# Optimization experiments

Measured on AMD Instinct MI355X. Metric: run time of the kernel, lower is better.

## Reference

```python
import jax, jax.numpy as jnp
import numpy as np

SLOPE = 25.0   # fast_sigmoid surrogate slope
THR = 1.0      # snntorch Leaky default threshold


@jax.custom_vjp
def spike(x):
    # Heaviside forward, fast-sigmoid surrogate backward
    return (x > 0).astype(x.dtype)

def _spike_fwd(x):
    return spike(x), x

def _spike_bwd(x, g):
    return (g / (SLOPE * jnp.abs(x) + 1.0) ** 2,)

spike.defvjp(_spike_fwd, _spike_bwd)


def conv2d(x, w, b):
    y = jax.lax.conv_general_dilated(
        x, w, window_strides=(1, 1), padding=((1, 1), (1, 1)),
        dimension_numbers=('NCHW', 'OIHW', 'NCHW'))
    return y + b[None, :, None, None]


def maxpool2(x):
    return jax.lax.reduce_window(x, -jnp.inf, jax.lax.max,
                                 (1, 1, 2, 2), (1, 1, 2, 2), 'VALID')


def bn_inf(x, g, b, m, v):
    # inference-mode BatchNorm2d, eps = 1e-5
    inv = g * jax.lax.rsqrt(v + 1e-5)
    return x * inv[None, :, None, None] + (b - m * inv)[None, :, None, None]


def lif_step(mem, inp, beta):
    # snntorch Leaky, reset_mechanism='subtract', learn_beta (clamped to [0,1])
    b = jnp.clip(beta, 0.0, 1.0)
    reset = jax.lax.stop_gradient((mem > THR).astype(mem.dtype))
    mem_new = b * mem + inp - reset * THR
    spk = spike(mem_new - THR)
    return spk, mem_new


def setup_inputs() -> dict:
    key = jax.random.key(0)
    ks = jax.random.split(key, 20)
    T, B, H, W = 25, 512, 100, 64   # T steps, batch, MAX_LEN, N_MELS
    NUM_CLASSES = 35
    FLAT = 32 * (H // 4) * (W // 4)  # 12800
    f32 = jnp.float32
    inp = {
        'x': jax.random.normal(ks[0], (T, B, H, W), f32),
        'conv1_w': jax.random.normal(ks[1], (16, 1, 3, 3), f32) * 0.2,
        'conv1_b': jnp.zeros((16,), f32),
        'bn1_g': jnp.ones((16,), f32),
        'bn1_b': jnp.zeros((16,), f32),
        'bn1_m': jax.random.normal(ks[2], (16,), f32) * 0.1,
        'bn1_v': jax.random.uniform(ks[3], (16,), f32) + 0.5,
        'conv2_w': jax.random.normal(ks[4], (32, 16, 3, 3), f32) * (1.0 / np.sqrt(16 * 9)),
        'conv2_b': jnp.zeros((32,), f32),
        'bn2_g': jnp.ones((32,), f32),
        'bn2_b': jnp.zeros((32,), f32),
        'bn2_m': jax.random.normal(ks[5], (32,), f32) * 0.1,
        'bn2_v': jax.random.uniform(ks[6], (32,), f32) + 0.5,
        'fc1_w': jax.random.normal(ks[7], (256, FLAT), f32) * (1.0 / np.sqrt(FLAT)),
        'fc1_b': jnp.zeros((256,), f32),
        'fc2_w': jax.random.normal(ks[8], (128, 256), f32) * (1.0 / np.sqrt(256)),
        'fc2_b': jnp.zeros((128,), f32),
        'fc3_w': jax.random.normal(ks[9], (NUM_CLASSES, 128), f32) * (1.0 / np.sqrt(128)),
        'fc3_b': jnp.zeros((NUM_CLASSES,), f32),
        'beta1': jnp.float32(0.9),
        'beta2': jnp.float32(0.9),
        'beta3': jnp.float32(0.9),
    }
    return inp


def reference(x, conv1_w, conv1_b, bn1_g, bn1_b, bn1_m, bn1_v,
              conv2_w, conv2_b, bn2_g, bn2_b, bn2_m, bn2_v,
              fc1_w, fc1_b, fc2_w, fc2_b, fc3_w, fc3_b,
              beta1, beta2, beta3):
    T, B = x.shape[0], x.shape[1]
    # CNN runs once on the time-averaged input
    x_mean = jnp.mean(x, axis=0)[:, None]          # (B, 1, H, W)
    f = maxpool2(jax.nn.relu(bn_inf(conv2d(x_mean, conv1_w, conv1_b), bn1_g, bn1_b, bn1_m, bn1_v)))
    f = maxpool2(jax.nn.relu(bn_inf(conv2d(f, conv2_w, conv2_b), bn2_g, bn2_b, bn2_m, bn2_v)))
    feat = f.reshape(B, -1)                        # (B, FLAT)
    # fc1 input is the same every step (dropout = identity in eval)
    cur1 = feat @ fc1_w.T + fc1_b                  # (B, 256)

    m1 = jnp.zeros((B, fc1_w.shape[0]), x.dtype)
    m2 = jnp.zeros((B, fc2_w.shape[0]), x.dtype)
    m3 = jnp.zeros((B, fc3_w.shape[0]), x.dtype)

    def step(carry, _):
        m1, m2, m3 = carry
        spk1, m1 = lif_step(m1, cur1, beta1)
        spk2, m2 = lif_step(m2, spk1 @ fc2_w.T + fc2_b, beta2)
        spk3, m3 = lif_step(m3, spk2 @ fc3_w.T + fc3_b, beta3)
        return (m1, m2, m3), spk3

    _, out = jax.lax.scan(step, (m1, m2, m3), None, length=T)
    return out                                     # (T, B, NUM_CLASSES)
```

## Files before the change

### kernel.cpp

```cpp
#include <hip/hip_runtime.h>

#define N_P1    (512*16*50*32)
#define N_FEAT  (512*12800)
#define N_PART  (32*512*256)

#define WS_P1    0
#define WS_FEAT  (WS_P1 + N_P1)
#define WS_PART  (WS_FEAT + N_FEAT)
#define WS_S1    0
#define WS_IN2   3276800
#define WS_S2    4915200
#define WS_IN3   6553600

__global__ __launch_bounds__(384) void conv1_kernel(const float* __restrict__ x,
                                                    const float* __restrict__ w1,
                                                    const float* __restrict__ cb1,
                                                    const float* __restrict__ g1,
                                                    const float* __restrict__ bb1,
                                                    const float* __restrict__ m1g,
                                                    const float* __restrict__ v1,
                                                    float* __restrict__ p1) {
    __shared__ float xs[22 * 66];
    __shared__ float w1s[144];
    __shared__ float sh1s[16];
    const int b = blockIdx.x, s = blockIdx.y;
    const int tid = threadIdx.x;
    if (tid < 144) {
        int c = tid / 9;
        float inv = g1[c] * rsqrtf(v1[c] + 1e-5f);
        w1s[tid] = w1[tid] * inv;
    }
    if (tid >= 144 && tid < 160) {
        int c = tid - 144;
        float inv = g1[c] * rsqrtf(v1[c] + 1e-5f);
        sh1s[c] = cb1[c] * inv + bb1[c] - m1g[c] * inv;
    }
    if (tid >= 160 && tid < 204) {
        int q = tid - 160;
        xs[(q >> 1) * 66 + (q & 1) * 65] = 0.f;
    }
    const int r0 = s * 20 - 1;
    const size_t TSTR = (size_t)512 * 6400;
    if (tid < 352) {
        int lr = tid >> 4, cq = tid & 15;
        int gr = r0 + lr;
        float4 a0 = make_float4(0.f, 0.f, 0.f, 0.f), a1 = a0, a2 = a0, a3 = a0;
        if (gr >= 0 && gr < 100) {
            const float* px = x + (size_t)b * 6400 + gr * 64 + cq * 4;
            #pragma unroll
            for (int tt = 0; tt < 24; tt += 4) {
                float4 v0 = *(const float4*)(px + (size_t)(tt + 0) * TSTR);
                float4 v1_ = *(const float4*)(px + (size_t)(tt + 1) * TSTR);
                float4 v2_ = *(const float4*)(px + (size_t)(tt + 2) * TSTR);
                float4 v3 = *(const float4*)(px + (size_t)(tt + 3) * TSTR);
                a0.x += v0.x; a0.y += v0.y; a0.z += v0.z; a0.w += v0.w;
                a1.x += v1_.x; a1.y += v1_.y; a1.z += v1_.z; a1.w += v1_.w;
                a2.x += v2_.x; a2.y += v2_.y; a2.z += v2_.z; a2.w += v2_.w;
                a3.x += v3.x; a3.y += v3.y; a3.z += v3.z; a3.w += v3.w;
            }
            float4 v = *(const float4*)(px + (size_t)24 * TSTR);
            a0.x += v.x; a0.y += v.y; a0.z += v.z; a0.w += v.w;
        }
        const float sc = 1.0f / 25.0f;
        float* d = &xs[lr * 66 + 1 + cq * 4];
        d[0] = (a0.x + a1.x + a2.x + a3.x) * sc;
        d[1] = (a0.y + a1.y + a2.y + a3.y) * sc;
        d[2] = (a0.z + a1.z + a2.z + a3.z) * sc;
        d[3] = (a0.w + a1.w + a2.w + a3.w) * sc;
    }
    __syncthreads();
    if (tid < 320) {
        int phl = tid >> 5, pw = tid & 31;
        int ph = s * 10 + phl;
        float win[4][4];
        #pragma unroll
        for (int a = 0; a < 4; ++a)
            #pragma unroll
            for (int c2 = 0; c2 < 4; ++c2)
                win[a][c2] = xs[(2 * phl + a) * 66 + 2 * pw + c2];
        #pragma unroll 1
        for (int c = 0; c < 16; ++c) {
            float s00 = 0.f, s01 = 0.f, s10 = 0.f, s11 = 0.f;
            #pragma unroll
            for (int dh = 0; dh < 3; ++dh)
                #pragma unroll
                for (int dw = 0; dw < 3; ++dw) {
                    float w = w1s[c * 9 + dh * 3 + dw];
                    s00 = fmaf(win[dh][dw],         w, s00);
                    s01 = fmaf(win[dh][dw + 1],     w, s01);
                    s10 = fmaf(win[dh + 1][dw],     w, s10);
                    s11 = fmaf(win[dh + 1][dw + 1], w, s11);
                }
            float m = fmaxf(fmaxf(s00, s01), fmaxf(s10, s11));
            float val = fmaxf(m + sh1s[c], 0.f);
            p1[(((size_t)b * 16 + c) * 50 + ph) * 32 + pw] = val;
        }
    }
}

__global__ __launch_bounds__(320) void conv2_kernel(const float* __restrict__ p1,
                                                    const float* __restrict__ w2g,
                                                    const float* __restrict__ cb2,
                                                    const float* __restrict__ g2,
                                                    const float* __restrict__ bb2,
                                                    const float* __restrict__ m2g,
                                                    const float* __restrict__ v2,
                                                    float* __restrict__ feat) {
    __shared__ float ins[16 * 12 * 36];
    __shared__ float wl[16 * 9 * 32];
    __shared__ float sh2s[32];
    const int b = blockIdx.x, s = blockIdx.y;
    const int tid = threadIdx.x;
    const int chg = tid & 15, q = (tid >> 4) & 3, phl = tid >> 6;
    const int ph = s * 5 + phl;

    for (int i = tid; i < 192; i += 320) {
        int ci = i / 12, lr = i - ci * 12;
        int gr = s * 10 - 1 + lr;
        float* dst = &ins[(ci * 12 + lr) * 36];
        if (gr >= 0 && gr < 50) {
            const float* src = p1 + (((size_t)b * 16 + ci) * 50 + gr) * 32;
            float4 v0 = *(const float4*)src;
            dst[0] = 0.f; dst[1] = v0.x; dst[2] = v0.y; dst[3] = v0.z;
            #pragma unroll
            for (int qq = 1; qq < 8; ++qq) {
                float4 v = *(const float4*)(src + 4 * qq - 1);
                *(float4*)(dst + 4 * qq) = v;
            }
            dst[32] = src[31];
            dst[33] = 0.f; dst[34] = 0.f; dst[35] = 0.f;
        } else {
            #pragma unroll
            for (int qq = 0; qq < 9; ++qq) *(float4*)(dst + 4 * qq) = make_float4(0.f, 0.f, 0.f, 0.f);
        }
    }
    for (int i = tid; i < 4608; i += 320) {
        int c = i / 144, rem = i - c * 144;
        float inv = g2[c] * rsqrtf(v2[c] + 1e-5f);
        wl[rem * 32 + c] = w2g[i] * inv;
    }
    if (tid < 32) {
        float inv = g2[tid] * rsqrtf(v2[tid] + 1e-5f);
        sh2s[tid] = cb2[tid] * inv + bb2[tid] - m2g[tid] * inv;
    }
    __syncthreads();

    float acc[2][2][8];
    #pragma unroll
    for (int c = 0; c < 2; ++c)
        #pragma unroll
        for (int a = 0; a < 2; ++a)
            #pragma unroll
            for (int xx = 0; xx < 8; ++xx) acc[c][a][xx] = 0.f;
    const int xb = q * 8;
    #pragma unroll 1
    for (int ci = 0; ci < 16; ++ci) {
        float2 wv[9];
        #pragma unroll
        for (int t = 0; t < 9; ++t)
            wv[t] = *(const float2*)&wl[(ci * 9 + t) * 32 + 2 * chg];
        #pragma unroll
        for (int lr4 = 0; lr4 < 4; ++lr4) {
            const float* row = &ins[(ci * 12 + (2 * phl + lr4)) * 36 + xb];
            float v[10];
            float4 t0 = *(const float4*)&row[0];
            float4 t1 = *(const float4*)&row[4];
            float2 t2 = *(const float2*)&row[8];
            v[0]=t0.x; v[1]=t0.y; v[2]=t0.z; v[3]=t0.w;
            v[4]=t1.x; v[5]=t1.y; v[6]=t1.z; v[7]=t1.w;
            v[8]=t2.x; v[9]=t2.y;
            #pragma unroll
            for (int a = 0; a < 2; ++a) {
                const int dh = lr4 - a;
                if (dh >= 0 && dh <= 2) {
                    #pragma unroll
                    for (int dw = 0; dw < 3; ++dw) {
                        float w0 = wv[dh * 3 + dw].x;
                        float w1 = wv[dh * 3 + dw].y;
                        #pragma unroll
                        for (int xx = 0; xx < 8; ++xx) {
                            acc[0][a][xx] = fmaf(v[xx + dw], w0, acc[0][a][xx]);
                            acc[1][a][xx] = fmaf(v[xx + dw], w1, acc[1][a][xx]);
                        }
                    }
                }
            }
        }
    }
    #pragma unroll
    for (int ch = 0; ch < 2; ++ch) {
        const int c = 2 * chg + ch;
        const float sh = sh2s[c];
        #pragma unroll
        for (int p = 0; p < 4; ++p) {
            float m = fmaxf(fmaxf(acc[ch][0][2 * p], acc[ch][0][2 * p + 1]),
                            fmaxf(acc[ch][1][2 * p], acc[ch][1][2 * p + 1]));
            float val = fmaxf(m + sh, 0.f);
            feat[(((size_t)b * 32 + c) * 25 + ph) * 16 + q * 4 + p] = val;
        }
    }
}

__global__ __launch_bounds__(256) void fc1_kernel(const float* __restrict__ feat,
                                                  const float* __restrict__ w,
                                                  float* __restrict__ part) {
    __shared__ float As[16 * 136];
    __shared__ float Bs[16 * 136];
    const int bx = blockIdx.x, by = blockIdx.y, bz = blockIdx.z;
    const int tid = threadIdx.x;
    const int tm = tid >> 4, tn = tid & 15;
    const int r = tid >> 2, cq = tid & 3;
    const int m0 = bx * 128, n0 = by * 128;
    const size_t aBase = (size_t)(m0 + r) * 12800 + bz * 400 + cq * 4;
    const size_t bBase = (size_t)(n0 + r) * 12800 + bz * 400 + cq * 4;
    float acc[8][8] = {};
    float4 a0 = *(const float4*)(feat + aBase);
    float4 a1 = *(const float4*)(feat + aBase + (size_t)64 * 12800);
    float4 b0 = *(const float4*)(w    + bBase);
    float4 b1 = *(const float4*)(w    + bBase + (size_t)64 * 12800);

    for (int kt = 0; kt < 25; ++kt) {
        __syncthreads();
        As[(cq * 4 + 0) * 136 + r]      = a0.x; As[(cq * 4 + 1) * 136 + r]      = a0.y;
        As[(cq * 4 + 2) * 136 + r]      = a0.z; As[(cq * 4 + 3) * 136 + r]      = a0.w;
        As[(cq * 4 + 0) * 136 + 64 + r] = a1.x; As[(cq * 4 + 1) * 136 + 64 + r] = a1.y;
        As[(cq * 4 + 2) * 136 + 64 + r] = a1.z; As[(cq * 4 + 3) * 136 + 64 + r] = a1.w;
        Bs[(cq * 4 + 0) * 136 + r]      = b0.x; Bs[(cq * 4 + 1) * 136 + r]      = b0.y;
        Bs[(cq * 4 + 2) * 136 + r]      = b0.z; Bs[(cq * 4 + 3) * 136 + r]      = b0.w;
        Bs[(cq * 4 + 0) * 136 + 64 + r] = b1.x; Bs[(cq * 4 + 1) * 136 + 64 + r] = b1.y;
        Bs[(cq * 4 + 2) * 136 + 64 + r] = b1.z; Bs[(cq * 4 + 3) * 136 + 64 + r] = b1.w;
        __syncthreads();
        if (kt < 24) {
            const int o = (kt + 1) * 16;
            a0 = *(const float4*)(feat + aBase + o);
            a1 = *(const float4*)(feat + aBase + (size_t)64 * 12800 + o);
            b0 = *(const float4*)(w    + bBase + o);
            b1 = *(const float4*)(w    + bBase + (size_t)64 * 12800 + o);
        }
        #pragma unroll
        for (int kk = 0; kk < 16; ++kk) {
            float4 av0 = *(const float4*)&As[kk * 136 + tm * 8];
            float4 av1 = *(const float4*)&As[kk * 136 + tm * 8 + 4];
            float4 bv0 = *(const float4*)&Bs[kk * 136 + tn * 8];
            float4 bv1 = *(const float4*)&Bs[kk * 136 + tn * 8 + 4];
            float a_[8] = {av0.x, av0.y, av0.z, av0.w, av1.x, av1.y, av1.z, av1.w};
            float b_[8] = {bv0.x, bv0.y, bv0.z, bv0.w, bv1.x, bv1.y, bv1.z, bv1.w};
            #pragma unroll
            for (int i = 0; i < 8; ++i)
                #pragma unroll
                for (int j = 0; j < 8; ++j)
                    acc[i][j] = fmaf(a_[i], b_[j], acc[i][j]);
        }
    }
    #pragma unroll
    for (int i = 0; i < 8; ++i) {
        float* dst = &part[(size_t)bz * 131072 + (size_t)(m0 + tm * 8 + i) * 256 + n0 + tn * 8];
        *(float4*)dst       = make_float4(acc[i][0], acc[i][1], acc[i][2], acc[i][3]);
        *(float4*)(dst + 4) = make_float4(acc[i][4], acc[i][5], acc[i][6], acc[i][7]);
    }
}

__global__ __launch_bounds__(256) void lif1_kernel(const float* __restrict__ part,
                                                   const float* __restrict__ b1g,
                                                   const float* __restrict__ pb1,
                                                   float* __restrict__ S1) {
    const int i = blockIdx.x * 256 + threadIdx.x;
    const int k = i & 255;
    float cu = b1g[k];
    #pragma unroll 8
    for (int z = 0; z < 32; ++z) cu += part[(size_t)z * 131072 + i];
    const float be = fminf(fmaxf(pb1[0], 0.f), 1.f);
    float m = 0.f;
    #pragma unroll
    for (int t = 0; t < 25; ++t) {
        float r = (m > 1.f) ? 1.f : 0.f;
        m = fmaf(be, m, cu) - r;
        S1[(size_t)t * 131072 + i] = (m > 1.f) ? 1.f : 0.f;
    }
}

__global__ __launch_bounds__(256) void fc2g_kernel(const float* __restrict__ S1,
                                                   const float* __restrict__ w2g,
                                                   const float* __restrict__ b2g,
                                                   float* __restrict__ in2) {
    __shared__ float As[16 * 36];
    __shared__ float Bs[16 * 136];
    const int m0 = blockIdx.x * 32;
    const int tid = threadIdx.x;
    const int tm = tid >> 4, tn = tid & 15;
    const int ra = tid >> 2, cqa = tid & 3;
    const int rb = tid >> 1, kb = (tid & 1) * 8;
    float acc[2][8] = {};
    float4 av = make_float4(0.f, 0.f, 0.f, 0.f);
    if (tid < 128) av = *(const float4*)&S1[(size_t)(m0 + ra) * 256 + cqa * 4];
    float4 bv0 = *(const float4*)&w2g[rb * 256 + kb];
    float4 bv1 = *(const float4*)&w2g[rb * 256 + kb + 4];

    for (int kt = 0; kt < 16; ++kt) {
        __syncthreads();
        if (tid < 128) {
            As[(cqa * 4 + 0) * 36 + ra] = av.x; As[(cqa * 4 + 1) * 36 + ra] = av.y;
            As[(cqa * 4 + 2) * 36 + ra] = av.z; As[(cqa * 4 + 3) * 36 + ra] = av.w;
        }
        Bs[(kb + 0) * 136 + rb] = bv0.x; Bs[(kb + 1) * 136 + rb] = bv0.y;
        Bs[(kb + 2) * 136 + rb] = bv0.z; Bs[(kb + 3) * 136 + rb] = bv0.w;
        Bs[(kb + 4) * 136 + rb] = bv1.x; Bs[(kb + 5) * 136 + rb] = bv1.y;
        Bs[(kb + 6) * 136 + rb] = bv1.z; Bs[(kb + 7) * 136 + rb] = bv1.w;
        __syncthreads();
        if (kt < 15) {
            const int o = (kt + 1) * 16;
            if (tid < 128) av = *(const float4*)&S1[(size_t)(m0 + ra) * 256 + o + cqa * 4];
            bv0 = *(const float4*)&w2g[rb * 256 + o + kb];
            bv1 = *(const float4*)&w2g[rb * 256 + o + kb + 4];
        }
        #pragma unroll
        for (int kk = 0; kk < 16; ++kk) {
            float2 a2 = *(const float2*)&As[kk * 36 + tm * 2];
            float4 bw0 = *(const float4*)&Bs[kk * 136 + tn * 8];
            float4 bw1 = *(const float4*)&Bs[kk * 136 + tn * 8 + 4];
            float b_[8] = {bw0.x, bw0.y, bw0.z, bw0.w, bw1.x, bw1.y, bw1.z, bw1.w};
            #pragma unroll
            for (int j = 0; j < 8; ++j) {
                acc[0][j] = fmaf(a2.x, b_[j], acc[0][j]);
                acc[1][j] = fmaf(a2.y, b_[j], acc[1][j]);
            }
        }
    }
    float4 bb0 = *(const float4*)&b2g[tn * 8];
    float4 bb1 = *(const float4*)&b2g[tn * 8 + 4];
    #pragma unroll
    for (int i = 0; i < 2; ++i) {
        float* dst = &in2[(size_t)(m0 + tm * 2 + i) * 128 + tn * 8];
        *(float4*)dst       = make_float4(acc[i][0] + bb0.x, acc[i][1] + bb0.y,
                                          acc[i][2] + bb0.z, acc[i][3] + bb0.w);
        *(float4*)(dst + 4) = make_float4(acc[i][4] + bb1.x, acc[i][5] + bb1.y,
                                          acc[i][6] + bb1.z, acc[i][7] + bb1.w);
    }
}

__global__ __launch_bounds__(256) void lif2_kernel(const float* __restrict__ in2,
                                                   const float* __restrict__ pb2,
                                                   float* __restrict__ S2) {
    const int i = blockIdx.x * 256 + threadIdx.x;
    const float be = fminf(fmaxf(pb2[0], 0.f), 1.f);
    float m = 0.f;
    #pragma unroll
    for (int t = 0; t < 25; ++t) {
        float r = (m > 1.f) ? 1.f : 0.f;
        m = fmaf(be, m, in2[(size_t)t * 65536 + i]) - r;
        S2[(size_t)t * 65536 + i] = (m > 1.f) ? 1.f : 0.f;
    }
}

__global__ __launch_bounds__(256) void fc3g_kernel(const float* __restrict__ S2,
                                                   const float* __restrict__ w3g,
                                                   const float* __restrict__ b3g,
                                                   float* __restrict__ in3) {
    __shared__ float As[16 * 36];
    __shared__ float Bs[16 * 48];
    const int m0 = blockIdx.x * 32;
    const int tid = threadIdx.x;
    const int tm = tid >> 4, tn = tid & 15;
    float acc[2][3] = {};
    for (int kt = 0; kt < 8; ++kt) {
        __syncthreads();
        if (tid < 128) {
            int r = tid >> 2, cq = tid & 3;
            float4 av = *(const float4*)&S2[(size_t)(m0 + r) * 128 + kt * 16 + cq * 4];
            As[(cq * 4 + 0) * 36 + r] = av.x; As[(cq * 4 + 1) * 36 + r] = av.y;
            As[(cq * 4 + 2) * 36 + r] = av.z; As[(cq * 4 + 3) * 36 + r] = av.w;
        }
        for (int i = tid; i < 560; i += 256) {
            int kk = i / 35, c = i - kk * 35;
            Bs[kk * 48 + c] = w3g[c * 128 + kt * 16 + kk];
        }
        __syncthreads();
        #pragma unroll
        for (int kk = 0; kk < 16; ++kk) {
            float2 a2 = *(const float2*)&As[kk * 36 + tm * 2];
            float w0 = Bs[kk * 48 + tn];
            float w1 = Bs[kk * 48 + tn + 16];
            float w2 = Bs[kk * 48 + tn + 32];
            acc[0][0] = fmaf(a2.x, w0, acc[0][0]); acc[1][0] = fmaf(a2.y, w0, acc[1][0]);
            acc[0][1] = fmaf(a2.x, w1, acc[0][1]); acc[1][1] = fmaf(a2.y, w1, acc[1][1]);
            acc[0][2] = fmaf(a2.x, w2, acc[0][2]); acc[1][2] = fmaf(a2.y, w2, acc[1][2]);
        }
    }
    const float bias0 = b3g[tn];
    const float bias1 = b3g[tn + 16];
    const float bias2 = (tn < 3) ? b3g[tn + 32] : 0.f;
    #pragma unroll
    for (int i = 0; i < 2; ++i) {
        const size_t row = (size_t)(m0 + tm * 2 + i) * 35;
        in3[row + tn]      = acc[i][0] + bias0;
        in3[row + tn + 16] = acc[i][1] + bias1;
        if (tn < 3) in3[row + tn + 32] = acc[i][2] + bias2;
    }
}

__global__ __launch_bounds__(256) void lif3_kernel(const float* __restrict__ in3,
                                                   const float* __restrict__ pb3,
                                                   float* __restrict__ out) {
    const int i = blockIdx.x * 256 + threadIdx.x;
    if (i >= 17920) return;
    const float be = fminf(fmaxf(pb3[0], 0.f), 1.f);
    float m = 0.f;
    #pragma unroll
    for (int t = 0; t < 25; ++t) {
        float r = (m > 1.f) ? 1.f : 0.f;
        m = fmaf(be, m, in3[(size_t)t * 17920 + i]) - r;
        out[(size_t)t * 17920 + i] = (m > 1.f) ? 1.f : 0.f;
    }
}

extern "C" void kernel_launch(void* const* d_in, const int* in_sizes, int n_in,
                              void* d_out, int out_size, void* d_ws, size_t ws_size,
                              hipStream_t stream) {
    const float* x     = (const float*)d_in[0];
    const float* c1w   = (const float*)d_in[1];
    const float* c1b   = (const float*)d_in[2];
    const float* bn1g  = (const float*)d_in[3];
    const float* bn1b  = (const float*)d_in[4];
    const float* bn1m  = (const float*)d_in[5];
    const float* bn1v  = (const float*)d_in[6];
    const float* c2w   = (const float*)d_in[7];
    const float* c2b   = (const float*)d_in[8];
    const float* bn2g  = (const float*)d_in[9];
    const float* bn2b  = (const float*)d_in[10];
    const float* bn2m  = (const float*)d_in[11];
    const float* bn2v  = (const float*)d_in[12];
    const float* fc1w  = (const float*)d_in[13];
    const float* fc1b  = (const float*)d_in[14];
    const float* fc2w  = (const float*)d_in[15];
    const float* fc2b  = (const float*)d_in[16];
    const float* fc3w  = (const float*)d_in[17];
    const float* fc3b  = (const float*)d_in[18];
    const float* beta1 = (const float*)d_in[19];
    const float* beta2 = (const float*)d_in[20];
    const float* beta3 = (const float*)d_in[21];
    float* ws  = (float*)d_ws;
    float* out = (float*)d_out;

    conv1_kernel<<<dim3(512, 5), 384, 0, stream>>>(x, c1w, c1b, bn1g, bn1b, bn1m, bn1v,
                                                   ws + WS_P1);
    conv2_kernel<<<dim3(512, 5), 320, 0, stream>>>(ws + WS_P1, c2w, c2b, bn2g, bn2b, bn2m, bn2v,
                                                   ws + WS_FEAT);
    fc1_kernel<<<dim3(4, 2, 32), 256, 0, stream>>>(ws + WS_FEAT, fc1w, ws + WS_PART);
    lif1_kernel<<<512, 256, 0, stream>>>(ws + WS_PART, fc1b, beta1, ws + WS_S1);
    fc2g_kernel<<<400, 256, 0, stream>>>(ws + WS_S1, fc2w, fc2b, ws + WS_IN2);
    lif2_kernel<<<256, 256, 0, stream>>>(ws + WS_IN2, beta2, ws + WS_S2);
    fc3g_kernel<<<400, 256, 0, stream>>>(ws + WS_S2, fc3w, fc3b, ws + WS_IN3);
    lif3_kernel<<<70, 256, 0, stream>>>(ws + WS_IN3, beta3, out);
}
```

Baseline: 300.4 us.

## Retile fc1 to full-N 128x256 tiles with 64-way split-K, nontemporal input loads

The fc1 GEMM now gives each block a full 256-wide N tile with a 16x8 micro-tile per thread. K is split 64 ways (200 per block) instead of 32, so the launch stays at 256 blocks while each feature row is read once per block rather than twice. The B shared-memory layout is padded (stride 10 per 8 columns) to reduce bank conflicts. conv1 reads the large time-series input with nontemporal vector loads to avoid polluting cache, and the workspace layout is reshuffled to hold the larger partial buffer. The costs are 64 partial sums to reduce in lif1, more registers per thread (launch bounds set to one block), and more partial-sum memory traffic.

```diff
diff --git a/kernel.cpp b/kernel.cpp
--- a/kernel.cpp
+++ b/kernel.cpp
@@ -1,16 +1,14 @@
 #include <hip/hip_runtime.h>
 
-#define N_P1    (512*16*50*32)
-#define N_FEAT  (512*12800)
-#define N_PART  (32*512*256)
+typedef float f4nt __attribute__((ext_vector_type(4)));
 
 #define WS_P1    0
-#define WS_FEAT  (WS_P1 + N_P1)
-#define WS_PART  (WS_FEAT + N_FEAT)
-#define WS_S1    0
-#define WS_IN2   3276800
-#define WS_S2    4915200
-#define WS_IN3   6553600
+#define WS_FEAT  13107200
+#define WS_PART  0
+#define WS_S1    8388608
+#define WS_IN2   11665408
+#define WS_S2    13303808
+#define WS_IN3   14942208
 
 __global__ __launch_bounds__(384) void conv1_kernel(const float* __restrict__ x,
                                                     const float* __restrict__ w1,
@@ -44,29 +42,24 @@
     if (tid < 352) {
         int lr = tid >> 4, cq = tid & 15;
         int gr = r0 + lr;
-        float4 a0 = make_float4(0.f, 0.f, 0.f, 0.f), a1 = a0, a2 = a0, a3 = a0;
+        f4nt a0 = {0.f, 0.f, 0.f, 0.f}, a1 = a0, a2 = a0, a3 = a0;
         if (gr >= 0 && gr < 100) {
             const float* px = x + (size_t)b * 6400 + gr * 64 + cq * 4;
             #pragma unroll
             for (int tt = 0; tt < 24; tt += 4) {
-                float4 v0 = *(const float4*)(px + (size_t)(tt + 0) * TSTR);
-                float4 v1_ = *(const float4*)(px + (size_t)(tt + 1) * TSTR);
-                float4 v2_ = *(const float4*)(px + (size_t)(tt + 2) * TSTR);
-                float4 v3 = *(const float4*)(px + (size_t)(tt + 3) * TSTR);
-                a0.x += v0.x; a0.y += v0.y; a0.z += v0.z; a0.w += v0.w;
-                a1.x += v1_.x; a1.y += v1_.y; a1.z += v1_.z; a1.w += v1_.w;
-                a2.x += v2_.x; a2.y += v2_.y; a2.z += v2_.z; a2.w += v2_.w;
-                a3.x += v3.x; a3.y += v3.y; a3.z += v3.z; a3.w += v3.w;
+                f4nt v0 = __builtin_nontemporal_load((const f4nt*)(px + (size_t)(tt + 0) * TSTR));
+                f4nt v1_ = __builtin_nontemporal_load((const f4nt*)(px + (size_t)(tt + 1) * TSTR));
+                f4nt v2_ = __builtin_nontemporal_load((const f4nt*)(px + (size_t)(tt + 2) * TSTR));
+                f4nt v3 = __builtin_nontemporal_load((const f4nt*)(px + (size_t)(tt + 3) * TSTR));
+                a0 += v0; a1 += v1_; a2 += v2_; a3 += v3;
             }
-            float4 v = *(const float4*)(px + (size_t)24 * TSTR);
-            a0.x += v.x; a0.y += v.y; a0.z += v.z; a0.w += v.w;
+            f4nt v = __builtin_nontemporal_load((const f4nt*)(px + (size_t)24 * TSTR));
+            a0 += v;
         }
         const float sc = 1.0f / 25.0f;
+        f4nt sm = (a0 + a1 + a2 + a3) * sc;
         float* d = &xs[lr * 66 + 1 + cq * 4];
-        d[0] = (a0.x + a1.x + a2.x + a3.x) * sc;
-        d[1] = (a0.y + a1.y + a2.y + a3.y) * sc;
-        d[2] = (a0.z + a1.z + a2.z + a3.z) * sc;
-        d[3] = (a0.w + a1.w + a2.w + a3.w) * sc;
+        d[0] = sm.x; d[1] = sm.y; d[2] = sm.z; d[3] = sm.w;
     }
     __syncthreads();
     if (tid < 320) {
@@ -201,60 +194,62 @@
     }
 }
 
-__global__ __launch_bounds__(256) void fc1_kernel(const float* __restrict__ feat,
-                                                  const float* __restrict__ w,
-                                                  float* __restrict__ part) {
-    __shared__ float As[16 * 136];
-    __shared__ float Bs[16 * 136];
-    const int bx = blockIdx.x, by = blockIdx.y, bz = blockIdx.z;
+__global__ __launch_bounds__(256, 1) void fc1_kernel(const float* __restrict__ feat,
+                                                     const float* __restrict__ w,
+                                                     float* __restrict__ part) {
+    __shared__ float As[8 * 136];
+    __shared__ float Bs[8 * 320];
+    const int bx = blockIdx.x, bz = blockIdx.y;
     const int tid = threadIdx.x;
-    const int tm = tid >> 4, tn = tid & 15;
-    const int r = tid >> 2, cq = tid & 3;
-    const int m0 = bx * 128, n0 = by * 128;
-    const size_t aBase = (size_t)(m0 + r) * 12800 + bz * 400 + cq * 4;
-    const size_t bBase = (size_t)(n0 + r) * 12800 + bz * 400 + cq * 4;
-    float acc[8][8] = {};
-    float4 a0 = *(const float4*)(feat + aBase);
-    float4 a1 = *(const float4*)(feat + aBase + (size_t)64 * 12800);
-    float4 b0 = *(const float4*)(w    + bBase);
-    float4 b1 = *(const float4*)(w    + bBase + (size_t)64 * 12800);
-
-    for (int kt = 0; kt < 25; ++kt) {
-        __syncthreads();
-        As[(cq * 4 + 0) * 136 + r]      = a0.x; As[(cq * 4 + 1) * 136 + r]      = a0.y;
-        As[(cq * 4 + 2) * 136 + r]      = a0.z; As[(cq * 4 + 3) * 136 + r]      = a0.w;
-        As[(cq * 4 + 0) * 136 + 64 + r] = a1.x; As[(cq * 4 + 1) * 136 + 64 + r] = a1.y;
-        As[(cq * 4 + 2) * 136 + 64 + r] = a1.z; As[(cq * 4 + 3) * 136 + 64 + r] = a1.w;
-        Bs[(cq * 4 + 0) * 136 + r]      = b0.x; Bs[(cq * 4 + 1) * 136 + r]      = b0.y;
-        Bs[(cq * 4 + 2) * 136 + r]      = b0.z; Bs[(cq * 4 + 3) * 136 + r]      = b0.w;
-        Bs[(cq * 4 + 0) * 136 + 64 + r] = b1.x; Bs[(cq * 4 + 1) * 136 + 64 + r] = b1.y;
-        Bs[(cq * 4 + 2) * 136 + 64 + r] = b1.z; Bs[(cq * 4 + 3) * 136 + 64 + r] = b1.w;
-        __syncthreads();
-        if (kt < 24) {
-            const int o = (kt + 1) * 16;
-            a0 = *(const float4*)(feat + aBase + o);
-            a1 = *(const float4*)(feat + aBase + (size_t)64 * 12800 + o);
-            b0 = *(const float4*)(w    + bBase + o);
-            b1 = *(const float4*)(w    + bBase + (size_t)64 * 12800 + o);
-        }
-        #pragma unroll
-        for (int kk = 0; kk < 16; ++kk) {
-            float4 av0 = *(const float4*)&As[kk * 136 + tm * 8];
-            float4 av1 = *(const float4*)&As[kk * 136 + tm * 8 + 4];
-            float4 bv0 = *(const float4*)&Bs[kk * 136 + tn * 8];
-            float4 bv1 = *(const float4*)&Bs[kk * 136 + tn * 8 + 4];
-            float a_[8] = {av0.x, av0.y, av0.z, av0.w, av1.x, av1.y, av1.z, av1.w};
-            float b_[8] = {bv0.x, bv0.y, bv0.z, bv0.w, bv1.x, bv1.y, bv1.z, bv1.w};
-            #pragma unroll
-            for (int i = 0; i < 8; ++i)
+    const int tm = tid >> 5, tn = tid & 31;
+    const int m0 = bx * 128;
+    const int k0 = bz * 200;
+    const int ar = tid >> 1, ac4 = (tid & 1) * 4;
+    const int br = tid >> 1, bh = (tid & 1) * 4;
+    const int gb0 = (br >> 3) * 10 + (br & 7);
+    const int gb1 = ((br + 128) >> 3) * 10 + (br & 7);
+
+    float acc[16][8] = {};
+    float4 aP  = *(const float4*)(feat + (size_t)(m0 + ar) * 12800 + k0 + ac4);
+    float4 bP0 = *(const float4*)(w + (size_t)br * 12800 + k0 + bh);
+    float4 bP1 = *(const float4*)(w + (size_t)(br + 128) * 12800 + k0 + bh);
+
+    for (int st = 0; st < 25; ++st) {
+        __syncthreads();
+        As[(ac4 + 0) * 136 + ar] = aP.x; As[(ac4 + 1) * 136 + ar] = aP.y;
+        As[(ac4 + 2) * 136 + ar] = aP.z; As[(ac4 + 3) * 136 + ar] = aP.w;
+        Bs[(bh + 0) * 320 + gb0] = bP0.x; Bs[(bh + 1) * 320 + gb0] = bP0.y;
+        Bs[(bh + 2) * 320 + gb0] = bP0.z; Bs[(bh + 3) * 320 + gb0] = bP0.w;
+        Bs[(bh + 0) * 320 + gb1] = bP1.x; Bs[(bh + 1) * 320 + gb1] = bP1.y;
+        Bs[(bh + 2) * 320 + gb1] = bP1.z; Bs[(bh + 3) * 320 + gb1] = bP1.w;
+        __syncthreads();
+        if (st < 24) {
+            const int o = k0 + (st + 1) * 8;
+            aP  = *(const float4*)(feat + (size_t)(m0 + ar) * 12800 + o + ac4);
+            bP0 = *(const float4*)(w + (size_t)br * 12800 + o + bh);
+            bP1 = *(const float4*)(w + (size_t)(br + 128) * 12800 + o + bh);
+        }
+        #pragma unroll
+        for (int kk = 0; kk < 8; ++kk) {
+            float4 a0 = *(const float4*)&As[kk * 136 + tm * 16];
+            float4 a1 = *(const float4*)&As[kk * 136 + tm * 16 + 4];
+            float4 a2 = *(const float4*)&As[kk * 136 + tm * 16 + 8];
+            float4 a3 = *(const float4*)&As[kk * 136 + tm * 16 + 12];
+            float4 b0 = *(const float4*)&Bs[kk * 320 + tn * 10];
+            float4 b1 = *(const float4*)&Bs[kk * 320 + tn * 10 + 4];
+            float a_[16] = {a0.x, a0.y, a0.z, a0.w, a1.x, a1.y, a1.z, a1.w,
+                            a2.x, a2.y, a2.z, a2.w, a3.x, a3.y, a3.z, a3.w};
+            float b_[8]  = {b0.x, b0.y, b0.z, b0.w, b1.x, b1.y, b1.z, b1.w};
+            #pragma unroll
+            for (int i = 0; i < 16; ++i)
                 #pragma unroll
                 for (int j = 0; j < 8; ++j)
                     acc[i][j] = fmaf(a_[i], b_[j], acc[i][j]);
         }
     }
     #pragma unroll
-    for (int i = 0; i < 8; ++i) {
-        float* dst = &part[(size_t)bz * 131072 + (size_t)(m0 + tm * 8 + i) * 256 + n0 + tn * 8];
+    for (int i = 0; i < 16; ++i) {
+        float* dst = &part[(size_t)bz * 131072 + (size_t)(m0 + tm * 16 + i) * 256 + tn * 8];
         *(float4*)dst       = make_float4(acc[i][0], acc[i][1], acc[i][2], acc[i][3]);
         *(float4*)(dst + 4) = make_float4(acc[i][4], acc[i][5], acc[i][6], acc[i][7]);
     }
@@ -268,7 +263,7 @@
     const int k = i & 255;
     float cu = b1g[k];
     #pragma unroll 8
-    for (int z = 0; z < 32; ++z) cu += part[(size_t)z * 131072 + i];
+    for (int z = 0; z < 64; ++z) cu += part[(size_t)z * 131072 + i];
     const float be = fminf(fmaxf(pb1[0], 0.f), 1.f);
     float m = 0.f;
     #pragma unroll
@@ -445,7 +440,7 @@
                                                    ws + WS_P1);
     conv2_kernel<<<dim3(512, 5), 320, 0, stream>>>(ws + WS_P1, c2w, c2b, bn2g, bn2b, bn2m, bn2v,
                                                    ws + WS_FEAT);
-    fc1_kernel<<<dim3(4, 2, 32), 256, 0, stream>>>(ws + WS_FEAT, fc1w, ws + WS_PART);
+    fc1_kernel<<<dim3(4, 64), 256, 0, stream>>>(ws + WS_FEAT, fc1w, ws + WS_PART);
     lif1_kernel<<<512, 256, 0, stream>>>(ws + WS_PART, fc1b, beta1, ws + WS_S1);
     fc2g_kernel<<<400, 256, 0, stream>>>(ws + WS_S1, fc2w, fc2b, ws + WS_IN2);
     lif2_kernel<<<256, 256, 0, stream>>>(ws + WS_IN2, beta2, ws + WS_S2);
```

Result: no change. 301.5 us (+0.4%).
